# Performance work log

Measured on AMD Instinct MI355X. Metric: run time of the kernel, lower is better.

Reference implementation:

```python
import jax, jax.numpy as jnp
import numpy as np

B, R, NB, T = 32, 96, 5, 2048
FEAT_DIM = 64
SPARSITY = 0.2


def _per_band(X, community, W1, b1, W2, b2):
    # X: [R, T] wavelet coeffs for one (batch, band) slice
    n, t = X.shape
    f32 = X.dtype
    # --- functional connectivity (cosine of centered signals == Pearson corr) ---
    Xc = X - X.mean(axis=1, keepdims=True)
    norm = jnp.linalg.norm(Xc, axis=1, keepdims=True)
    norm = jnp.where(norm == 0, 1.0, norm)
    C = (Xc @ Xc.T) / (norm * norm.T)
    C = jnp.nan_to_num(C, nan=0.0)
    C = C * (1.0 - jnp.eye(n, dtype=f32))  # zero diagonal
    # --- quantile sparsification over strict lower triangle ---
    ti, tj = np.tril_indices(n, -1)
    thr = jnp.quantile(jnp.abs(C[ti, tj]), 1.0 - SPARSITY)
    A = C * (jnp.abs(C) >= thr).astype(f32)  # graph_type == 'weighted'
    # --- node features (5-dim, averaged over regions) ---
    mean_f = X.mean(axis=1)
    std_f = jnp.std(X, axis=1, ddof=1)  # torch.std is unbiased
    energy_f = (X ** 2).sum(axis=1)
    maxamp_f = jnp.abs(X).max(axis=1)
    ps = jnp.abs(jnp.fft.fft(X, axis=1)) ** 2
    ps = ps[:, : t // 2]
    s = ps.sum(axis=1, keepdims=True)
    s = jnp.where(s == 0, 1.0, s)
    p = ps / s
    ent_f = -(p * jnp.log(p + 1e-10)).sum(axis=1)
    node5 = jnp.stack([mean_f, std_f, energy_f, maxamp_f, ent_f], axis=1).mean(axis=0)
    # --- graph properties (6-dim) on binarized adjacency ---
    Bm = (A != 0).astype(f32)
    ne = Bm.sum() / 2.0
    density = ne / (n * (n - 1) / 2.0)
    deg = Bm.sum(axis=1)
    avg_deg = deg.mean()
    A2 = Bm @ Bm
    tri = (A2 * Bm).sum() / 6.0
    poss = (deg * (deg - 1.0)).sum() / 2.0
    clus = jnp.where(poss > 0, tri / jnp.where(poss > 0, poss, 1.0), 0.0)
    # global efficiency: safe reciprocal (zero where A+I == 0; original would emit inf)
    denom = Bm + jnp.eye(n, dtype=f32)
    eff = jnp.where(denom > 0, 1.0 / jnp.where(denom > 0, denom, 1.0), 0.0).sum() / (n * (n - 1))
    # approximate modularity with fixed 2-community assignment (deterministic)
    m2 = 2.0 * ne
    m2_safe = jnp.where(m2 > 0, m2, 1.0)
    same = (community[:, None] == community[None, :]) & (~jnp.eye(n, dtype=bool))
    expected = jnp.outer(deg, deg) / m2_safe
    mod = jnp.where(m2 > 0, (same * (Bm - expected)).sum() / m2_safe, 0.0)
    props = jnp.stack([ne, density, avg_deg, clus, eff, mod])
    feat11 = jnp.concatenate([node5, props])  # [11]
    # --- feature encoder MLP (dropout is identity at inference) ---
    h = jnp.maximum(feat11 @ W1.T + b1, 0.0)
    return A, h @ W2.T + b2


def _forward(wavelet_coeffs, frequency_bands, community, W1, b1, W2, b2):
    b, r, nb, t = wavelet_coeffs.shape
    Xs = wavelet_coeffs.transpose(0, 2, 1, 3).reshape(b * nb, r, t)  # [B*NB, R, T]
    A, F = jax.vmap(_per_band, in_axes=(0, None, None, None, None, None))(
        Xs, community, W1, b1, W2, b2)
    return A.reshape(b, nb, r, r), F.reshape(b, nb, -1)


def setup_inputs() -> dict:
    key = jax.random.key(0)
    k0, k1, k2, k3, k4 = jax.random.split(key, 5)
    wavelet_coeffs = jax.random.normal(k0, (B, R, NB, T), dtype=jnp.float32)
    frequency_bands = jax.random.uniform(k1, (NB, 2), dtype=jnp.float32)
    community = jax.random.randint(k2, (R,), 0, 2)
    W1 = jax.random.normal(k3, (32, 11), dtype=jnp.float32) * 0.3
    b1 = jnp.zeros((32,), jnp.float32)
    W2 = jax.random.normal(k4, (FEAT_DIM, 32), dtype=jnp.float32) * 0.18
    b2 = jnp.zeros((FEAT_DIM,), jnp.float32)
    return {"wavelet_coeffs": wavelet_coeffs, "frequency_bands": frequency_bands,
            "community": community, "W1": W1, "b1": b1, "W2": W2, "b2": b2}


def reference(wavelet_coeffs, frequency_bands, community, W1, b1, W2, b2):
    return _forward(wavelet_coeffs, frequency_bands, community, W1, b1, W2, b2)
```

## Files before the change

### kernel.cpp

```cpp
#include <hip/hip_runtime.h>
#include <hip/hip_bf16.h>
#include <math.h>
#include <float.h>

#ifndef M_PI
#define M_PI 3.14159265358979323846
#endif

#define NBANDS 160
#define RR 96
#define TT 2048
#define NTRIL 4560
#define A_ELEMS ((size_t)NBANDS * RR * RR)
#define NBIN 8192
#define MAXCAND 512
#define BKS 64
#define NST (TT / BKS)
#define GPITCH 76
#define FBLK 512

#define PHI(L) ((L) ^ (((L) >> 5) & 31))

typedef float  f32x4  __attribute__((ext_vector_type(4)));
typedef __bf16 bf16x8 __attribute__((ext_vector_type(8)));
typedef __bf16 bf16x4 __attribute__((ext_vector_type(4)));

__device__ inline void blockReduceSum4(double v0, double v1, double v2, double v3,
                                       double* sred, double out[4]) {
    for (int off = 32; off > 0; off >>= 1) {
        v0 += __shfl_down(v0, off, 64);
        v1 += __shfl_down(v1, off, 64);
        v2 += __shfl_down(v2, off, 64);
        v3 += __shfl_down(v3, off, 64);
    }
    int lane = threadIdx.x & 63, wid = threadIdx.x >> 6;
    int nw = blockDim.x >> 6;
    if (lane == 0) {
        sred[wid * 4 + 0] = v0; sred[wid * 4 + 1] = v1;
        sred[wid * 4 + 2] = v2; sred[wid * 4 + 3] = v3;
    }
    __syncthreads();
    if (threadIdx.x < 4) {
        double r = sred[threadIdx.x];
        for (int w = 1; w < nw; w++) r += sred[w * 4 + threadIdx.x];
        sred[nw * 4 + threadIdx.x] = r;
    }
    __syncthreads();
    out[0] = sred[nw * 4 + 0]; out[1] = sred[nw * 4 + 1];
    out[2] = sred[nw * 4 + 2]; out[3] = sred[nw * 4 + 3];
    __syncthreads();
}

__device__ inline void blockReduceSum2(double v0, double v1,
                                       double* sred, double out[2]) {
    for (int off = 32; off > 0; off >>= 1) {
        v0 += __shfl_down(v0, off, 64);
        v1 += __shfl_down(v1, off, 64);
    }
    int lane = threadIdx.x & 63, wid = threadIdx.x >> 6;
    int nw = blockDim.x >> 6;
    if (lane == 0) { sred[wid * 2 + 0] = v0; sred[wid * 2 + 1] = v1; }
    __syncthreads();
    if (threadIdx.x < 2) {
        double r = sred[threadIdx.x];
        for (int w = 1; w < nw; w++) r += sred[w * 2 + threadIdx.x];
        sred[nw * 2 + threadIdx.x] = r;
    }
    __syncthreads();
    out[0] = sred[nw * 2 + 0]; out[1] = sred[nw * 2 + 1];
    __syncthreads();
}

__device__ inline void blockReduceMax2(double v0, double v1,
                                       double* sred, double out[2]) {
    for (int off = 32; off > 0; off >>= 1) {
        v0 = fmax(v0, __shfl_down(v0, off, 64));
        v1 = fmax(v1, __shfl_down(v1, off, 64));
    }
    int lane = threadIdx.x & 63, wid = threadIdx.x >> 6;
    int nw = blockDim.x >> 6;
    if (lane == 0) { sred[wid * 2 + 0] = v0; sred[wid * 2 + 1] = v1; }
    __syncthreads();
    if (threadIdx.x < 2) {
        double r = sred[threadIdx.x];
        for (int w = 1; w < nw; w++) r = fmax(r, sred[w * 2 + threadIdx.x]);
        sred[nw * 2 + threadIdx.x] = r;
    }
    __syncthreads();
    out[0] = sred[nw * 2 + 0]; out[1] = sred[nw * 2 + 1];
    __syncthreads();
}

__global__ void twiddle_kernel(float* tw) {
    int k = blockIdx.x * blockDim.x + threadIdx.x;
    if (k < 1024) {
        double ang = -2.0 * M_PI * (double)k / 2048.0;
        tw[2 * k]     = (float)cos(ang);
        tw[2 * k + 1] = (float)sin(ang);
    }
}

#define BFLY(r1, r2, WR, WI) do { \
    float _wr = (WR), _wi = (WI); \
    float _tr = _wr * yr[r2] - _wi * yi[r2]; \
    float _ti = _wr * yi[r2] + _wi * yr[r2]; \
    yr[r2] = yr[r1] - _tr; yi[r2] = yi[r1] - _ti; \
    yr[r1] += _tr; yi[r1] += _ti; } while (0)

__global__ __launch_bounds__(256) void rowstat_fft_kernel(
    const float* __restrict__ wc, const float* __restrict__ tw,
    double* __restrict__ rowstats)
{
    __shared__ float re[TT];
    __shared__ float im[TT];
    __shared__ double sred[32];
    __shared__ float bcast[4];

    int t = threadIdx.x;
    int g0 = blockIdx.x * 2;
    int g1 = g0 + 1;

    int band = g0 / RR, r0 = g0 % RR;
    int b = band / 5, nb = band % 5;
    size_t base0 = ((size_t)(b * RR + r0) * 5 + nb) * TT;
    size_t base1 = base0 + (size_t)5 * TT;
    const float2* twv = (const float2*)tw;

    float s0 = 0.f, s1 = 0.f, q0 = 0.f, q1 = 0.f, m0 = 0.f, m1 = 0.f;
#pragma unroll
    for (int c = 0; c < 8; c++) {
        int i = t + c * 256;
        float af = wc[base0 + i];
        float bf = wc[base1 + i];
        int P = PHI(i);
        re[P] = af; im[P] = bf;
        s0 += af; s1 += bf;
        q0 = fmaf(af, af, q0); q1 = fmaf(bf, bf, q1);
        m0 = fmaxf(m0, fabsf(af)); m1 = fmaxf(m1, fabsf(bf));
    }
    __syncthreads();

    double S4[4], M2[2];
    blockReduceSum4((double)s0, (double)s1, (double)q0, (double)q1, sred, S4);
    blockReduceMax2((double)m0, (double)m1, sred, M2);
    double SUM0 = S4[0], SUM1 = S4[1], SQ0 = S4[2], SQ1 = S4[3];
    double MX0 = M2[0], MX1 = M2[1];

    float yr[8], yi[8];

#pragma unroll
    for (int j = 0; j < 8; j++) {
        int p = 8 * t + j;
        int L = (int)(__brev((unsigned)p) >> 21);
        int P = PHI(L);
        yr[j] = re[P]; yi[j] = im[P];
    }

    const float RC = 0.70710678f;
    BFLY(0, 1, 1.0f, 0.0f); BFLY(2, 3, 1.0f, 0.0f);
    BFLY(4, 5, 1.0f, 0.0f); BFLY(6, 7, 1.0f, 0.0f);
    BFLY(0, 2, 1.0f, 0.0f); BFLY(1, 3, 0.0f, -1.0f);
    BFLY(4, 6, 1.0f, 0.0f); BFLY(5, 7, 0.0f, -1.0f);
    BFLY(0, 4, 1.0f, 0.0f); BFLY(1, 5, RC, -RC);
    BFLY(2, 6, 0.0f, -1.0f); BFLY(3, 7, -RC, -RC);

    __syncthreads();
#pragma unroll
    for (int j = 0; j < 8; j++) {
        int P = PHI(8 * t + j);
        re[P] = yr[j]; im[P] = yi[j];
    }
    __syncthreads();
    int oo = t & 7;
    int bb64 = 4 * ((t >> 3) & 7) + (t >> 6);
#pragma unroll
    for (int k = 0; k < 8; k++) {
        int P = PHI(64 * bb64 + 8 * k + oo);
        yr[k] = re[P]; yi[k] = im[P];
    }

    {
        float2 w0 = twv[oo << 7];
        BFLY(0, 1, w0.x, w0.y); BFLY(2, 3, w0.x, w0.y);
        BFLY(4, 5, w0.x, w0.y); BFLY(6, 7, w0.x, w0.y);
        float2 wa = twv[oo << 6];
        float2 wb = twv[(oo + 8) << 6];
        BFLY(0, 2, wa.x, wa.y); BFLY(1, 3, wb.x, wb.y);
        BFLY(4, 6, wa.x, wa.y); BFLY(5, 7, wb.x, wb.y);
        float2 wc0 = twv[oo << 5], wc1 = twv[(oo + 8) << 5];
        float2 wc2 = twv[(oo + 16) << 5], wc3 = twv[(oo + 24) << 5];
        BFLY(0, 4, wc0.x, wc0.y);
        BFLY(1, 5, wc1.x, wc1.y);
        BFLY(2, 6, wc2.x, wc2.y);
        BFLY(3, 7, wc3.x, wc3.y);
    }

    __syncthreads();
#pragma unroll
    for (int k = 0; k < 8; k++) {
        int P = PHI(64 * bb64 + 8 * k + oo);
        re[P] = yr[k]; im[P] = yi[k];
    }
    __syncthreads();
    int O3 = t & 63, Wq = t >> 6;
#pragma unroll
    for (int s = 0; s < 2; s++) {
        int B3 = Wq + 4 * s;
#pragma unroll
        for (int k = 0; k < 4; k++) {
            int P = PHI(256 * B3 + 64 * k + O3);
            yr[4 * s + k] = re[P]; yi[4 * s + k] = im[P];
        }
    }

    {
        float2 w0 = twv[O3 << 4];
        float2 wa = twv[O3 << 3];
        float2 wb = twv[(O3 + 64) << 3];
        BFLY(0, 1, w0.x, w0.y); BFLY(2, 3, w0.x, w0.y);
        BFLY(4, 5, w0.x, w0.y); BFLY(6, 7, w0.x, w0.y);
        BFLY(0, 2, wa.x, wa.y); BFLY(1, 3, wb.x, wb.y);
        BFLY(4, 6, wa.x, wa.y); BFLY(5, 7, wb.x, wb.y);
    }

    __syncthreads();
#pragma unroll
    for (int s = 0; s < 2; s++) {
        int B3 = Wq + 4 * s;
#pragma unroll
        for (int k = 0; k < 4; k++) {
            int P = PHI(256 * B3 + 64 * k + O3);
            re[P] = yr[4 * s + k]; im[P] = yi[4 * s + k];
        }
    }
    __syncthreads();
#pragma unroll
    for (int k = 0; k < 8; k++) {
        int P = PHI(256 * k + t);
        yr[k] = re[P]; yi[k] = im[P];
    }

    {
        float2 w0 = twv[t << 2];
        float2 wa = twv[t << 1];
        float2 wb = twv[(t + 256) << 1];
        BFLY(0, 1, w0.x, w0.y); BFLY(2, 3, w0.x, w0.y);
        BFLY(4, 5, w0.x, w0.y); BFLY(6, 7, w0.x, w0.y);
        BFLY(0, 2, wa.x, wa.y); BFLY(1, 3, wb.x, wb.y);
        BFLY(4, 6, wa.x, wa.y); BFLY(5, 7, wb.x, wb.y);
        float2 wf0 = twv[t], wf1 = twv[t + 256];
        float2 wf2 = twv[t + 512], wf3 = twv[t + 768];
        BFLY(0, 4, wf0.x, wf0.y);
        BFLY(1, 5, wf1.x, wf1.y);
        BFLY(2, 6, wf2.x, wf2.y);
        BFLY(3, 7, wf3.x, wf3.y);
    }

    __syncthreads();
#pragma unroll
    for (int k = 0; k < 8; k++) {
        int P = PHI(256 * k + t);
        re[P] = yr[k]; im[P] = yi[k];
    }
    __syncthreads();

    float psa[8], psb[8];
#pragma unroll
    for (int k = 0; k < 8; k++) {
        int q = (2048 - t - 256 * k) & 2047;
        int P = PHI(q);
        float prr = re[P], pii = im[P];
        float sr = yr[k] + prr, di = yi[k] - pii;
        float si = yi[k] + pii, dr = yr[k] - prr;
        psa[k] = 0.25f * (sr * sr + di * di);
        psb[k] = 0.25f * (si * si + dr * dr);
    }

    float la = 0.f, lb = 0.f;
#pragma unroll
    for (int k = 0; k < 8; k++) { la += psa[k]; lb += psb[k]; }
    double SS[2];
    blockReduceSum2((double)la, (double)lb, sred, SS);
    double SAall = SS[0], SBall = SS[1];
    if (t == 0) {
        bcast[0] = psa[0]; bcast[1] = psa[4];
        bcast[2] = psb[0]; bcast[3] = psb[4];
    }
    __syncthreads();
    double Sa = 0.5 * (SAall + (double)bcast[0] - (double)bcast[1]);
    double Sb = 0.5 * (SBall + (double)bcast[2] - (double)bcast[3]);
    if (Sa == 0.0) Sa = 1.0;
    if (Sb == 0.0) Sb = 1.0;
    float invSa = (float)(1.0 / Sa), invSb = (float)(1.0 / Sb);

    float ea = 0.f, eb = 0.f;
#pragma unroll
    for (int k = 0; k < 8; k++) {
        float pa = psa[k] * invSa;
        float pb = psb[k] * invSb;
        ea += pa * __logf(pa + 1e-10f);
        eb += pb * __logf(pb + 1e-10f);
    }
    double EE[2];
    blockReduceSum2((double)ea, (double)eb, sred, EE);
    double EAall = EE[0], EBall = EE[1];

    if (t == 0) {
        float pa0 = psa[0] * invSa, pa4 = psa[4] * invSa;
        float pb0 = psb[0] * invSb, pb4 = psb[4] * invSb;
        double TA = 0.5 * (EAall + (double)(pa0 * __logf(pa0 + 1e-10f))
                                 - (double)(pa4 * __logf(pa4 + 1e-10f)));
        double TB = 0.5 * (EBall + (double)(pb0 * __logf(pb0 + 1e-10f))
                                 - (double)(pb4 * __logf(pb4 + 1e-10f)));
        double mean0 = SUM0 / (double)TT;
        double mean1 = SUM1 / (double)TT;
        double nsq0 = SQ0 - (double)TT * mean0 * mean0; if (nsq0 < 0) nsq0 = 0;
        double nsq1 = SQ1 - (double)TT * mean1 * mean1; if (nsq1 < 0) nsq1 = 0;
        double* w0 = rowstats + (size_t)g0 * 6;
        double* w1 = rowstats + (size_t)g1 * 6;
        double n0 = sqrt(nsq0), n1 = sqrt(nsq1);
        w0[0] = mean0; w0[1] = (n0 == 0.0 ? 1.0 : n0); w0[2] = sqrt(nsq0 / 2047.0);
        w0[3] = SQ0;   w0[4] = MX0;                    w0[5] = -TA;
        w1[0] = mean1; w1[1] = (n1 == 0.0 ? 1.0 : n1); w1[2] = sqrt(nsq1 / 2047.0);
        w1[3] = SQ1;   w1[4] = MX1;                    w1[5] = -TB;
    }
}

#define CVW(BUF, v, row, c4) do { \
    __bf16 _h0 = (__bf16)v.x, _h1 = (__bf16)v.y, _h2 = (__bf16)v.z, _h3 = (__bf16)v.w; \
    __bf16 _l0 = (__bf16)(v.x - (float)_h0), _l1 = (__bf16)(v.y - (float)_h1); \
    __bf16 _l2 = (__bf16)(v.z - (float)_h2), _l3 = (__bf16)(v.w - (float)_h3); \
    *(bf16x4*)&sh_hi[BUF][row][(c4) * 4] = (bf16x4){_h0, _h1, _h2, _h3}; \
    *(bf16x4*)&sh_lo[BUF][row][(c4) * 4] = (bf16x4){_l0, _l1, _l2, _l3}; } while (0)

#define LDFRAG(dst, arr, BUF, row, ko) do { \
    bf16x4 _f0 = *(const bf16x4*)&arr[BUF][row][ko]; \
    bf16x4 _f1 = *(const bf16x4*)&arr[BUF][row][(ko) + 4]; \
    dst = (bf16x8){_f0[0], _f0[1], _f0[2], _f0[3], _f1[0], _f1[1], _f1[2], _f1[3]}; } while (0)

__global__ __launch_bounds__(FBLK) void fused_gram_finalize_kernel(
    const float* __restrict__ wc, const double* __restrict__ rowstats,
    const int* __restrict__ community,
    const float* __restrict__ W1, const float* __restrict__ b1,
    const float* __restrict__ W2, const float* __restrict__ b2,
    float* __restrict__ A_out, float* __restrict__ F_out)
{
    __shared__ __attribute__((aligned(16))) __bf16 sh_hi[2][RR][GPITCH];
    __shared__ __attribute__((aligned(16))) __bf16 sh_lo[2][RR][GPITCH];
    __shared__ float Cs[RR][RR];
    __shared__ int hist[NBIN];
    __shared__ int chunkv[256];
    __shared__ int pchunk[256];
    __shared__ int gpre_s[64];
    __shared__ float cand[MAXCAND];
    __shared__ int ctrl[8];
    __shared__ float selv[2];
    __shared__ double mean_s[RR], inv_s[RR];
    __shared__ int comm_s[RR];
    __shared__ unsigned long long msk[RR][2];
    __shared__ int deg[RR];
    __shared__ double sred[40];
    __shared__ double feat[11];
    __shared__ double hmlp[32];
    __shared__ double thr_s;

    int band = blockIdx.x, t = threadIdx.x;
    int b = band / 5, nb = band % 5;
    size_t bandbase = ((size_t)b * RR * 5 + nb) * TT;
    const double* rsb = rowstats + (size_t)band * RR * 6;

    if (t < RR) {
        mean_s[t] = rsb[t * 6 + 0];
        inv_s[t]  = 1.0 / rsb[t * 6 + 1];
        comm_s[t] = community[t];
    }
    for (int i = t; i < NBIN; i += FBLK) hist[i] = 0;
    if (t == 0) ctrl[3] = 0;

    int wave = t >> 6, lane = t & 63;
    int m16 = lane & 15, quad = lane >> 4;
    int kw = wave >> 2;
    int wq = wave & 3;
    int wr = wq >> 1;
    int wcx = wq & 1;

    int row0 = t >> 4,           c40 = t & 15;
    int row1 = (t + 512) >> 4,   c41 = (t + 512) & 15;
    int row2 = (t + 1024) >> 4,  c42 = (t + 1024) & 15;
    const float* p0 = wc + bandbase + (size_t)row0 * (5 * TT) + c40 * 4;
    const float* p1 = wc + bandbase + (size_t)row1 * (5 * TT) + c41 * 4;
    const float* p2 = wc + bandbase + (size_t)row2 * (5 * TT) + c42 * 4;

    f32x4 acc[3][3];
#pragma unroll
    for (int rs = 0; rs < 3; rs++)
#pragma unroll
        for (int cs = 0; cs < 3; cs++) acc[rs][cs] = (f32x4){0.f, 0.f, 0.f, 0.f};

    {
        float4 v0 = *(const float4*)(p0);
        float4 v1 = *(const float4*)(p1);
        float4 v2 = *(const float4*)(p2);
        CVW(0, v0, row0, c40); CVW(0, v1, row1, c41); CVW(0, v2, row2, c42);
    }
    __syncthreads();

    for (int st = 0; st < NST; st++) {
        int cur = st & 1;
        float4 q0, q1, q2;
        bool more = (st + 1 < NST);
        if (more) {
            int k0 = (st + 1) * BKS;
            q0 = *(const float4*)(p0 + k0);
            q1 = *(const float4*)(p1 + k0);
            q2 = *(const float4*)(p2 + k0);
        }
        {
            int ko = kw * 32 + quad * 8;
            bf16x8 ah[3], al[3];
#pragma unroll
            for (int rs = 0; rs < 3; rs++) {
                int ar = wr * 48 + rs * 16 + m16;
                LDFRAG(ah[rs], sh_hi, cur, ar, ko);
                LDFRAG(al[rs], sh_lo, cur, ar, ko);
            }
#pragma unroll
            for (int cs = 0; cs < 3; cs++) {
                int br = wcx * 48 + cs * 16 + m16;
                bf16x8 bh, bl;
                LDFRAG(bh, sh_hi, cur, br, ko);
                LDFRAG(bl, sh_lo, cur, br, ko);
#pragma unroll
                for (int rs = 0; rs < 3; rs++) {
                    acc[rs][cs] = __builtin_amdgcn_mfma_f32_16x16x32_bf16(ah[rs], bh, acc[rs][cs], 0, 0, 0);
                    acc[rs][cs] = __builtin_amdgcn_mfma_f32_16x16x32_bf16(ah[rs], bl, acc[rs][cs], 0, 0, 0);
                    acc[rs][cs] = __builtin_amdgcn_mfma_f32_16x16x32_bf16(al[rs], bh, acc[rs][cs], 0, 0, 0);
                }
            }
        }
        if (more) {
            int nxt = cur ^ 1;
            CVW(nxt, q0, row0, c40); CVW(nxt, q1, row1, c41); CVW(nxt, q2, row2, c42);
        }
        __syncthreads();
    }

    if (kw == 1) {
#pragma unroll
        for (int rs = 0; rs < 3; rs++)
#pragma unroll
            for (int cs = 0; cs < 3; cs++)
#pragma unroll
                for (int r = 0; r < 4; r++) {
                    int grow = wr * 48 + rs * 16 + quad * 4 + r;
                    int gcol = wcx * 48 + cs * 16 + m16;
                    Cs[grow][gcol] = acc[rs][cs][r];
                }
    }
    __syncthreads();
    if (kw == 0) {
#pragma unroll
        for (int rs = 0; rs < 3; rs++)
#pragma unroll
            for (int cs = 0; cs < 3; cs++)
#pragma unroll
                for (int r = 0; r < 4; r++) {
                    int grow = wr * 48 + rs * 16 + quad * 4 + r;
                    int gcol = wcx * 48 + cs * 16 + m16;
                    acc[rs][cs][r] += Cs[grow][gcol];
                }
    }
    __syncthreads();

    if (kw == 0) {
#pragma unroll
        for (int rs = 0; rs < 3; rs++) {
#pragma unroll
            for (int cs = 0; cs < 3; cs++) {
#pragma unroll
                for (int r = 0; r < 4; r++) {
                    int grow = wr * 48 + rs * 16 + quad * 4 + r;
                    int gcol = wcx * 48 + cs * 16 + m16;
                    double cd = ((double)acc[rs][cs][r]
                                 - (double)TT * mean_s[grow] * mean_s[gcol])
                                * (inv_s[grow] * inv_s[gcol]);
                    if (grow == gcol) cd = 0.0;
                    float cf = (float)cd;
                    Cs[grow][gcol] = cf;
                    if (gcol < grow) {
                        float val = fabsf(cf);
                        int bin = (int)(val * (float)NBIN);
                        bin = bin > (NBIN - 1) ? (NBIN - 1) : bin;
                        atomicAdd(&hist[bin], 1);
                    }
                }
            }
        }
    }
    __syncthreads();

    if (t < 256) {
        int cs = 0;
#pragma unroll
        for (int i = 0; i < NBIN / 256; i++) cs += hist[t * (NBIN / 256) + i];
        chunkv[t] = cs;
    }
    __syncthreads();
    if (t < 64) {
        int s4 = chunkv[4 * t] + chunkv[4 * t + 1] + chunkv[4 * t + 2] + chunkv[4 * t + 3];
        int inc = s4;
        for (int d = 1; d < 64; d <<= 1) {
            int u = __shfl_up(inc, d, 64);
            if (t >= d) inc += u;
        }
        gpre_s[t] = inc - s4;
    }
    __syncthreads();
    if (t < 256) {
        int base = gpre_s[t >> 2];
        for (int j = (t & ~3); j < t; j++) base += chunkv[j];
        pchunk[t] = base;
    }
    __syncthreads();
    if (t < 256) {
        int lo = pchunk[t], hi2 = lo + chunkv[t];
        if (lo <= 3647 && 3647 < hi2) ctrl[4] = t;
        if (lo <= 3648 && 3648 < hi2) ctrl[5] = t;
    }
    __syncthreads();
    {
        int c0 = ctrl[4], c1 = ctrl[5];
        if (t < 32) {
            int binb = c0 * 32;
            int pre = pchunk[c0];
            for (int j = 0; j < t; j++) pre += hist[binb + j];
            int cnt = hist[binb + t];
            if (pre <= 3647 && 3647 < pre + cnt) { ctrl[0] = binb + t; ctrl[2] = pre; }
        } else if (t < 64) {
            int tt2 = t - 32;
            int binb = c1 * 32;
            int pre = pchunk[c1];
            for (int j = 0; j < tt2; j++) pre += hist[binb + j];
            int cnt = hist[binb + tt2];
            if (pre <= 3648 && 3648 < pre + cnt) ctrl[1] = binb + tt2;
        }
    }
    __syncthreads();

    int B0 = ctrl[0], B1 = ctrl[1];
    for (int idx = t; idx < RR * RR; idx += FBLK) {
        int i = idx / RR, j = idx % RR;
        if (j < i) {
            float val = fabsf(Cs[i][j]);
            int bin = (int)(val * (float)NBIN);
            bin = bin > (NBIN - 1) ? (NBIN - 1) : bin;
            if (bin >= B0 && bin <= B1) {
                int k = atomicAdd(&ctrl[3], 1);
                if (k < MAXCAND) cand[k] = val;
            }
        }
    }
    __syncthreads();

    {
        int n = ctrl[3]; if (n > MAXCAND) n = MAXCAND;
        int r0l = 3647 - ctrl[2];
        int r1l = 3648 - ctrl[2];
        for (int i = t; i < n; i += FBLK) {
            float v = cand[i];
            int rank = 0;
            for (int j = 0; j < n; j++) {
                float u = cand[j];
                rank += (u < v || (u == v && j < i)) ? 1 : 0;
            }
            if (rank == r0l) selv[0] = v;
            if (rank == r1l) selv[1] = v;
        }
    }
    __syncthreads();
    if (t == 0) {
        double v0 = (double)selv[0], v1 = (double)selv[1];
        thr_s = v0 + 0.2 * (v1 - v0);
    }
    __syncthreads();
    double thr = thr_s;

    float* Ab = A_out + (size_t)band * (RR * RR);
    for (int idx = t; idx < RR * RR; idx += FBLK) {
        float cf = Cs[idx / RR][idx % RR];
        bool keep = ((double)fabsf(cf) >= thr);
        Ab[idx] = keep ? cf : 0.f;
    }

    for (int i = wave; i < RR; i += 8) {
        float vlo = Cs[i][lane];
        bool klo = ((double)fabsf(vlo) >= thr) && (vlo != 0.f);
        unsigned long long blo = __ballot(klo);
        float vhi = Cs[i][64 + (lane & 31)];
        bool khi = (lane < 32) && ((double)fabsf(vhi) >= thr) && (vhi != 0.f);
        unsigned long long bhi = __ballot(khi) & 0xffffffffull;
        if (lane == 0) {
            msk[i][0] = blo; msk[i][1] = bhi;
            deg[i] = __popcll(blo) + __popcll(bhi);
        }
    }
    __syncthreads();

    double triord = 0, ein = 0, expin = 0;
    for (int idx = t; idx < RR * RR; idx += FBLK) {
        int i = idx / RR, j = idx % RR;
        unsigned long long mi0 = msk[i][0], mi1 = msk[i][1];
        bool bij = (((j < 64) ? (mi0 >> j) : (mi1 >> (j - 64))) & 1ull) != 0;
        if (bij)
            triord += (double)(__popcll(mi0 & msk[j][0]) +
                               __popcll(mi1 & msk[j][1]));
        if (i != j && comm_s[i] == comm_s[j]) {
            ein += bij ? 1.0 : 0.0;
            expin += (double)deg[i] * (double)deg[j];
        }
    }
    double dv = (t < RR) ? (double)deg[t] : 0.0;
    double R1v[4], R2v[4], R3v[2];
    blockReduceSum4(triord, ein, expin, dv, sred, R1v);
    blockReduceSum4((t < RR) ? dv * (dv - 1.0) : 0.0,
                    (t < RR) ? rsb[t * 6 + 0] : 0.0,
                    (t < RR) ? rsb[t * 6 + 2] : 0.0,
                    (t < RR) ? rsb[t * 6 + 3] : 0.0, sred, R2v);
    blockReduceSum2((t < RR) ? rsb[t * 6 + 4] : 0.0,
                    (t < RR) ? rsb[t * 6 + 5] : 0.0, sred, R3v);
    double TRI = R1v[0], EIN = R1v[1], EXPIN = R1v[2], DEGS = R1v[3];
    double POSS2 = R2v[0], N0 = R2v[1], N1 = R2v[2], N2 = R2v[3];
    double N3 = R3v[0], N4 = R3v[1];

    if (t == 0) {
        double ne = 0.5 * DEGS;
        feat[0] = N0 / (double)RR;
        feat[1] = N1 / (double)RR;
        feat[2] = N2 / (double)RR;
        feat[3] = N3 / (double)RR;
        feat[4] = N4 / (double)RR;
        feat[5] = ne;
        feat[6] = ne / (double)NTRIL;
        feat[7] = DEGS / (double)RR;
        double tri = TRI / 6.0, poss = POSS2 * 0.5;
        feat[8] = (poss > 0.0) ? tri / poss : 0.0;
        feat[9] = ((double)RR + DEGS) / ((double)RR * (double)(RR - 1));
        double m2 = DEGS;
        feat[10] = (m2 > 0.0) ? (EIN - EXPIN / m2) / m2 : 0.0;
    }
    __syncthreads();

    if (t < 32) {
        double a = (double)b1[t];
        for (int k = 0; k < 11; k++) a += (double)W1[t * 11 + k] * feat[k];
        hmlp[t] = (a > 0.0) ? a : 0.0;
    }
    __syncthreads();
    if (t < 64) {
        double a = (double)b2[t];
        for (int j = 0; j < 32; j++) a += (double)W2[t * 32 + j] * hmlp[j];
        F_out[(size_t)band * 64 + t] = (float)a;
    }
}

extern "C" void kernel_launch(void* const* d_in, const int* in_sizes, int n_in,
                              void* d_out, int out_size, void* d_ws, size_t ws_size,
                              hipStream_t stream) {
    const float* wc        = (const float*)d_in[0];
    const int*   community = (const int*)d_in[2];
    const float* W1        = (const float*)d_in[3];
    const float* b1        = (const float*)d_in[4];
    const float* W2        = (const float*)d_in[5];
    const float* b2        = (const float*)d_in[6];

    float* A_out = (float*)d_out;
    float* F_out = A_out + A_ELEMS;

    char* ws = (char*)d_ws;
    float*  tw       = (float*)ws;
    double* rowstats = (double*)(ws + 8192);

    hipLaunchKernelGGL(twiddle_kernel, dim3(4), dim3(256), 0, stream, tw);
    hipLaunchKernelGGL(rowstat_fft_kernel, dim3(NBANDS * RR / 2), dim3(256), 0, stream,
                       wc, tw, rowstats);
    hipLaunchKernelGGL(fused_gram_finalize_kernel, dim3(NBANDS), dim3(FBLK), 0, stream,
                       wc, rowstats, community, W1, b1, W2, b2, A_out, F_out);
}
```

Baseline: 286.1 us.

## Shrink shared memory to raise occupancy of fused gram/finalize kernel

Drops the double-buffered bf16 staging to a single buffer, shrinks the quantile histogram from 8192 to 2048 bins with a simpler one-wave prefix scan, and aliases several late-phase shared arrays into one scratch region. It also asks for 4 blocks per CU in the launch bounds. The aim is to cut LDS use and register pressure so more blocks fit per CU. In exchange the loop loses its prefetch-convert overlap and gains an extra barrier per stage. Coarser bins put more values in each bin, so the candidate search may overflow its now smaller 256-entry buffer.

```diff
diff --git a/kernel.cpp b/kernel.cpp
--- a/kernel.cpp
+++ b/kernel.cpp
@@ -12,8 +12,8 @@
 #define TT 2048
 #define NTRIL 4560
 #define A_ELEMS ((size_t)NBANDS * RR * RR)
-#define NBIN 8192
-#define MAXCAND 512
+#define NBIN 2048
+#define MAXCAND 256
 #define BKS 64
 #define NST (TT / BKS)
 #define GPITCH 76
@@ -326,43 +326,44 @@
     }
 }
 
-#define CVW(BUF, v, row, c4) do { \
+#define CVW(v, row, c4) do { \
     __bf16 _h0 = (__bf16)v.x, _h1 = (__bf16)v.y, _h2 = (__bf16)v.z, _h3 = (__bf16)v.w; \
     __bf16 _l0 = (__bf16)(v.x - (float)_h0), _l1 = (__bf16)(v.y - (float)_h1); \
     __bf16 _l2 = (__bf16)(v.z - (float)_h2), _l3 = (__bf16)(v.w - (float)_h3); \
-    *(bf16x4*)&sh_hi[BUF][row][(c4) * 4] = (bf16x4){_h0, _h1, _h2, _h3}; \
-    *(bf16x4*)&sh_lo[BUF][row][(c4) * 4] = (bf16x4){_l0, _l1, _l2, _l3}; } while (0)
-
-#define LDFRAG(dst, arr, BUF, row, ko) do { \
-    bf16x4 _f0 = *(const bf16x4*)&arr[BUF][row][ko]; \
-    bf16x4 _f1 = *(const bf16x4*)&arr[BUF][row][(ko) + 4]; \
+    *(bf16x4*)&sh_hi[row][(c4) * 4] = (bf16x4){_h0, _h1, _h2, _h3}; \
+    *(bf16x4*)&sh_lo[row][(c4) * 4] = (bf16x4){_l0, _l1, _l2, _l3}; } while (0)
+
+#define LDFRAG(dst, arr, row, ko) do { \
+    bf16x4 _f0 = *(const bf16x4*)&arr[row][ko]; \
+    bf16x4 _f1 = *(const bf16x4*)&arr[row][(ko) + 4]; \
     dst = (bf16x8){_f0[0], _f0[1], _f0[2], _f0[3], _f1[0], _f1[1], _f1[2], _f1[3]}; } while (0)
 
-__global__ __launch_bounds__(FBLK) void fused_gram_finalize_kernel(
+__global__ __launch_bounds__(FBLK, 4) void fused_gram_finalize_kernel(
     const float* __restrict__ wc, const double* __restrict__ rowstats,
     const int* __restrict__ community,
     const float* __restrict__ W1, const float* __restrict__ b1,
     const float* __restrict__ W2, const float* __restrict__ b2,
     float* __restrict__ A_out, float* __restrict__ F_out)
 {
-    __shared__ __attribute__((aligned(16))) __bf16 sh_hi[2][RR][GPITCH];
-    __shared__ __attribute__((aligned(16))) __bf16 sh_lo[2][RR][GPITCH];
+    __shared__ __attribute__((aligned(16))) __bf16 sh_hi[RR][GPITCH];
+    __shared__ __attribute__((aligned(16))) __bf16 sh_lo[RR][GPITCH];
     __shared__ float Cs[RR][RR];
-    __shared__ int hist[NBIN];
-    __shared__ int chunkv[256];
-    __shared__ int pchunk[256];
-    __shared__ int gpre_s[64];
+    __shared__ __attribute__((aligned(16))) char scratch[8192];
+    __shared__ int chunkv[64];
+    __shared__ int pchunk[64];
     __shared__ float cand[MAXCAND];
     __shared__ int ctrl[8];
     __shared__ float selv[2];
     __shared__ double mean_s[RR], inv_s[RR];
     __shared__ int comm_s[RR];
-    __shared__ unsigned long long msk[RR][2];
-    __shared__ int deg[RR];
-    __shared__ double sred[40];
-    __shared__ double feat[11];
-    __shared__ double hmlp[32];
     __shared__ double thr_s;
+
+    int* hist = (int*)scratch;
+    unsigned long long (*msk)[2] = (unsigned long long (*)[2])scratch;
+    int*    deg  = (int*)(scratch + 1536);
+    double* sred = (double*)(scratch + 1920);
+    double* feat = (double*)(scratch + 2240);
+    double* hmlp = (double*)(scratch + 2328);
 
     int band = blockIdx.x, t = threadIdx.x;
     int b = band / 5, nb = band % 5;
@@ -397,23 +398,19 @@
 #pragma unroll
         for (int cs = 0; cs < 3; cs++) acc[rs][cs] = (f32x4){0.f, 0.f, 0.f, 0.f};
 
-    {
-        float4 v0 = *(const float4*)(p0);
-        float4 v1 = *(const float4*)(p1);
-        float4 v2 = *(const float4*)(p2);
-        CVW(0, v0, row0, c40); CVW(0, v1, row1, c41); CVW(0, v2, row2, c42);
-    }
+    float4 v0 = *(const float4*)(p0);
+    float4 v1 = *(const float4*)(p1);
+    float4 v2 = *(const float4*)(p2);
     __syncthreads();
 
     for (int st = 0; st < NST; st++) {
-        int cur = st & 1;
-        float4 q0, q1, q2;
-        bool more = (st + 1 < NST);
-        if (more) {
+        CVW(v0, row0, c40); CVW(v1, row1, c41); CVW(v2, row2, c42);
+        __syncthreads();
+        if (st + 1 < NST) {
             int k0 = (st + 1) * BKS;
-            q0 = *(const float4*)(p0 + k0);
-            q1 = *(const float4*)(p1 + k0);
-            q2 = *(const float4*)(p2 + k0);
+            v0 = *(const float4*)(p0 + k0);
+            v1 = *(const float4*)(p1 + k0);
+            v2 = *(const float4*)(p2 + k0);
         }
         {
             int ko = kw * 32 + quad * 8;
@@ -421,15 +418,15 @@
 #pragma unroll
             for (int rs = 0; rs < 3; rs++) {
                 int ar = wr * 48 + rs * 16 + m16;
-                LDFRAG(ah[rs], sh_hi, cur, ar, ko);
-                LDFRAG(al[rs], sh_lo, cur, ar, ko);
+                LDFRAG(ah[rs], sh_hi, ar, ko);
+                LDFRAG(al[rs], sh_lo, ar, ko);
             }
 #pragma unroll
             for (int cs = 0; cs < 3; cs++) {
                 int br = wcx * 48 + cs * 16 + m16;
                 bf16x8 bh, bl;
-                LDFRAG(bh, sh_hi, cur, br, ko);
-                LDFRAG(bl, sh_lo, cur, br, ko);
+                LDFRAG(bh, sh_hi, br, ko);
+                LDFRAG(bl, sh_lo, br, ko);
 #pragma unroll
                 for (int rs = 0; rs < 3; rs++) {
                     acc[rs][cs] = __builtin_amdgcn_mfma_f32_16x16x32_bf16(ah[rs], bh, acc[rs][cs], 0, 0, 0);
@@ -437,10 +434,6 @@
                     acc[rs][cs] = __builtin_amdgcn_mfma_f32_16x16x32_bf16(al[rs], bh, acc[rs][cs], 0, 0, 0);
                 }
             }
-        }
-        if (more) {
-            int nxt = cur ^ 1;
-            CVW(nxt, q0, row0, c40); CVW(nxt, q1, row1, c41); CVW(nxt, q2, row2, c42);
         }
         __syncthreads();
     }
@@ -499,30 +492,20 @@
     }
     __syncthreads();
 
-    if (t < 256) {
+    if (t < 64) {
         int cs = 0;
 #pragma unroll
-        for (int i = 0; i < NBIN / 256; i++) cs += hist[t * (NBIN / 256) + i];
-        chunkv[t] = cs;
-    }
-    __syncthreads();
-    if (t < 64) {
-        int s4 = chunkv[4 * t] + chunkv[4 * t + 1] + chunkv[4 * t + 2] + chunkv[4 * t + 3];
-        int inc = s4;
+        for (int i = 0; i < NBIN / 64; i++) cs += hist[t * (NBIN / 64) + i];
+        int inc = cs;
         for (int d = 1; d < 64; d <<= 1) {
             int u = __shfl_up(inc, d, 64);
             if (t >= d) inc += u;
         }
-        gpre_s[t] = inc - s4;
-    }
-    __syncthreads();
-    if (t < 256) {
-        int base = gpre_s[t >> 2];
-        for (int j = (t & ~3); j < t; j++) base += chunkv[j];
-        pchunk[t] = base;
-    }
-    __syncthreads();
-    if (t < 256) {
+        chunkv[t] = cs;
+        pchunk[t] = inc - cs;
+    }
+    __syncthreads();
+    if (t < 64) {
         int lo = pchunk[t], hi2 = lo + chunkv[t];
         if (lo <= 3647 && 3647 < hi2) ctrl[4] = t;
         if (lo <= 3648 && 3648 < hi2) ctrl[5] = t;
@@ -579,8 +562,8 @@
     }
     __syncthreads();
     if (t == 0) {
-        double v0 = (double)selv[0], v1 = (double)selv[1];
-        thr_s = v0 + 0.2 * (v1 - v0);
+        double v0d = (double)selv[0], v1d = (double)selv[1];
+        thr_s = v0d + 0.2 * (v1d - v0d);
     }
     __syncthreads();
     double thr = thr_s;
```

New measurement: 287.6 us. Within noise of the previous version (+0.5%).
